# Performance work log

Hardware: AMD Instinct MI355X
Metric: run time of the kernel (lower is better)

## Reference

```python
import jax, jax.numpy as jnp
import numpy as np

ALPHA = 0.2      # LeakyReLU negative slope
NEG_INF = -9e15  # mask value from the original module
EPS = 1e-8


def setup_inputs() -> dict:
    key = jax.random.key(0)
    k1, k2, k3, k4 = jax.random.split(key, 4)
    B, N, F_in, F_out = 8, 2048, 128, 64
    h = jax.random.normal(k1, (B, N, F_in), dtype=jnp.float32)
    u = jax.random.uniform(k2, (B, N, N), dtype=jnp.float32)
    adj = jnp.where(u > 0.9, u, 0.0)
    adj = jnp.maximum(adj, jnp.eye(N, dtype=jnp.float32)[None])
    # Xavier-uniform with gain 1.414 as in the torch init
    gain = 1.414
    bW = gain * np.sqrt(6.0 / (F_in + F_out))
    W = jax.random.uniform(k3, (F_in, F_out), jnp.float32, -bW, bW)
    ba = gain * np.sqrt(6.0 / (2 * F_out + 1))
    a = jax.random.uniform(k4, (2 * F_out, 1), jnp.float32, -ba, ba)
    return {"h": h, "adj": adj, "W": W, "a": a}


def reference(h, adj, W, a):
    # h: [B,N,Fin], adj: [B,N,N], W: [Fin,Fout], a: [2*Fout,1]
    F_out = W.shape[1]
    Wh = jnp.einsum('bnf,fo->bno', h, W)                      # [B,N,Fout]
    # Split-projection equivalent of cat([Wh_i, Wh_j]) @ a:
    # e[b,i,j] = leaky(Wh[b,i]@a1 + Wh[b,j]@a2)
    a1 = a[:F_out, 0]
    a2 = a[F_out:, 0]
    e = jax.nn.leaky_relu(
        (Wh @ a1)[:, :, None] + (Wh @ a2)[:, None, :],        # [B,N,N]
        negative_slope=ALPHA,
    )
    att = jnp.where(adj > 0, e, NEG_INF)
    att = jax.nn.softmax(att, axis=2)
    att = att * adj
    att = att / (jnp.sum(att, axis=2, keepdims=True) + EPS)
    h_prime = jnp.einsum('bij,bjo->bio', att, Wh)             # [B,N,Fout]
    return jax.nn.elu(h_prime)                                # concat=True -> ELU
```

## Files before the change

### kernel.cpp

```cpp
#include <hip/hip_runtime.h>
#include <hip/hip_bf16.h>
#include <stdint.h>

#define LRELU_ALPHA 0.2f

constexpr int BB = 8, NN = 2048, FIN = 128, FOUT = 64;

typedef __attribute__((ext_vector_type(8))) short short8;
typedef __attribute__((ext_vector_type(4))) float f32x4;

__device__ __forceinline__ ushort bf16rn(float f) {
    __hip_bfloat16 h = __float2bfloat16(f);
    return *reinterpret_cast<ushort*>(&h);
}

#define HS 132
__global__ __launch_bounds__(256) void k_gemm_hw(const float* __restrict__ h,
                                                 const float* __restrict__ W,
                                                 const float* __restrict__ a,
                                                 ushort* __restrict__ WhP,
                                                 float* __restrict__ s1,
                                                 float* __restrict__ s2,
                                                 float* __restrict__ pmax) {
    __shared__ float hs[64 * HS];
    __shared__ float smax[16];
    const int tid = threadIdx.x;
    const int base = blockIdx.x * 64;

    #pragma unroll
    for (int rep = 0; rep < 8; ++rep) {
        int flat4 = rep * 256 + tid;
        int row = flat4 >> 5, k4 = flat4 & 31;
        float4 v = *reinterpret_cast<const float4*>(h + (size_t)(base + row) * FIN + k4 * 4);
        *reinterpret_cast<float4*>(&hs[row * HS + k4 * 4]) = v;
    }
    __syncthreads();

    const int tr = tid >> 4;
    const int tc = tid & 15;
    float acc[4][4] = {};
    for (int k = 0; k < FIN; ++k) {
        float4 wv = *reinterpret_cast<const float4*>(W + (size_t)k * FOUT + tc * 4);
        #pragma unroll
        for (int r = 0; r < 4; ++r) {
            float hv = hs[(tr * 4 + r) * HS + k];
            acc[r][0] = fmaf(hv, wv.x, acc[r][0]);
            acc[r][1] = fmaf(hv, wv.y, acc[r][1]);
            acc[r][2] = fmaf(hv, wv.z, acc[r][2]);
            acc[r][3] = fmaf(hv, wv.w, acc[r][3]);
        }
    }

    const int b = base >> 11;
    const int jbase = base & 2047;
    #pragma unroll
    for (int r = 0; r < 4; ++r) {
        const int jloc = jbase + tr * 4 + r;
        const int e = jloc & 7;
        const int kgrp = (jloc >> 3) & 3;
        const int jblk = jloc >> 5;
        #pragma unroll
        for (int c = 0; c < 4; ++c) {
            const int col = tc * 4 + c;
            size_t off = ((((size_t)b * 64 + jblk) * 4 + (col >> 4)) * 64 + kgrp * 16 + (col & 15)) * 8 + e;
            WhP[off] = bf16rn(acc[r][c]);
        }
    }

    float a1c[4], a2c[4];
    #pragma unroll
    for (int c = 0; c < 4; ++c) {
        a1c[c] = a[tc * 4 + c];
        a2c[c] = a[FOUT + tc * 4 + c];
    }
    float maxp2 = -3.4e38f;
    #pragma unroll
    for (int r = 0; r < 4; ++r) {
        float p1 = acc[r][0] * a1c[0] + acc[r][1] * a1c[1] + acc[r][2] * a1c[2] + acc[r][3] * a1c[3];
        float p2 = acc[r][0] * a2c[0] + acc[r][1] * a2c[1] + acc[r][2] * a2c[2] + acc[r][3] * a2c[3];
        #pragma unroll
        for (int off = 1; off < 16; off <<= 1) {
            p1 += __shfl_xor(p1, off);
            p2 += __shfl_xor(p2, off);
        }
        if (tc == 0) {
            s1[base + tr * 4 + r] = p1;
            s2[base + tr * 4 + r] = p2;
            maxp2 = fmaxf(maxp2, p2);
        }
    }
    if (tc == 0) smax[tr] = maxp2;
    __syncthreads();
    if (tid == 0) {
        float m = smax[0];
        #pragma unroll
        for (int i = 1; i < 16; ++i) m = fmaxf(m, smax[i]);
        pmax[blockIdx.x] = m;
    }
}

struct Tile {
    float4 a0, a1;
    float4 v0, v1;
    short8 b0, b1, b2, b3;
};

__device__ __forceinline__ void proc8(const Tile& T, float s1i, float c,
                                      float& Sp, short8& af) {
    const float aa[8] = {T.a0.x, T.a0.y, T.a0.z, T.a0.w, T.a1.x, T.a1.y, T.a1.z, T.a1.w};
    const float ss[8] = {T.v0.x, T.v0.y, T.v0.z, T.v0.w, T.v1.x, T.v1.y, T.v1.z, T.v1.w};
    #pragma unroll
    for (int e = 0; e < 8; ++e) {
        float ev = s1i + ss[e];
        ev = ev > 0.f ? ev : LRELU_ALPHA * ev;
        float ex = __expf(ev - c);
        float wv = aa[e] > 0.f ? aa[e] * ex : 0.f;
        ushort ub = bf16rn(wv);
        Sp += __uint_as_float((uint32_t)ub << 16);
        af[e] = (short)ub;
    }
}

__global__ __launch_bounds__(256) void k_attn(const float* __restrict__ adj,
                                              const ushort* __restrict__ WhP,
                                              const float* __restrict__ s1,
                                              const float* __restrict__ s2,
                                              const float* __restrict__ pmax,
                                              float* __restrict__ out) {
    const int tid = threadIdx.x;
    const int l = tid & 63, w = tid >> 6;
    const int li = l & 15, lk = l >> 4;
    const int blk = blockIdx.x;
    const int b = blk >> 5;
    const int rowbase = blk * 64 + w * 16;
    const int row_i = rowbase + li;

    float m = -3.4e38f;
    #pragma unroll
    for (int t = 0; t < 4; ++t) m = fmaxf(m, pmax[l + 64 * t]);
    #pragma unroll
    for (int off = 32; off > 0; off >>= 1) m = fmaxf(m, __shfl_xor(m, off));

    const float s1i = s1[row_i];
    const float cp = s1i + m;
    const float c = cp > 0.f ? cp : LRELU_ALPHA * cp;

    const float* __restrict__ adjp = adj + (size_t)row_i * NN + lk * 8;
    const float* __restrict__ s2p  = s2 + (size_t)b * NN + lk * 8;
    const ushort* __restrict__ whp = WhP + (size_t)b * (64 * 4 * 64 * 8) + l * 8;

    f32x4 acc0 = {0.f, 0.f, 0.f, 0.f};
    f32x4 acc1 = {0.f, 0.f, 0.f, 0.f};
    f32x4 acc2 = {0.f, 0.f, 0.f, 0.f};
    f32x4 acc3 = {0.f, 0.f, 0.f, 0.f};
    float Sp = 0.f;

#define LOADT(T, jb) do {                                                     \
        (T).a0 = *reinterpret_cast<const float4*>(adjp + (jb) * 32);          \
        (T).a1 = *reinterpret_cast<const float4*>(adjp + (jb) * 32 + 4);      \
        (T).v0 = *reinterpret_cast<const float4*>(s2p + (jb) * 32);           \
        (T).v1 = *reinterpret_cast<const float4*>(s2p + (jb) * 32 + 4);       \
        const ushort* p_ = whp + (jb) * 2048;                                 \
        (T).b0 = *reinterpret_cast<const short8*>(p_);                        \
        (T).b1 = *reinterpret_cast<const short8*>(p_ + 512);                  \
        (T).b2 = *reinterpret_cast<const short8*>(p_ + 1024);                 \
        (T).b3 = *reinterpret_cast<const short8*>(p_ + 1536);                 \
    } while (0)

#define COMPUTE(T) do {                                                       \
        short8 af;                                                            \
        proc8((T), s1i, c, Sp, af);                                           \
        acc0 = __builtin_amdgcn_mfma_f32_16x16x32_bf16(af, (T).b0, acc0, 0, 0, 0); \
        acc1 = __builtin_amdgcn_mfma_f32_16x16x32_bf16(af, (T).b1, acc1, 0, 0, 0); \
        acc2 = __builtin_amdgcn_mfma_f32_16x16x32_bf16(af, (T).b2, acc2, 0, 0, 0); \
        acc3 = __builtin_amdgcn_mfma_f32_16x16x32_bf16(af, (T).b3, acc3, 0, 0, 0); \
    } while (0)

    Tile t0, t1;
    LOADT(t0, 0);
    LOADT(t1, 1);
    for (int jb = 0; jb < 64; jb += 2) {
        Tile n0, n1;
        if (jb + 2 < 64) {
            LOADT(n0, jb + 2);
            LOADT(n1, jb + 3);
        }
        COMPUTE(t0);
        COMPUTE(t1);
        t0 = n0;
        t1 = n1;
    }

    float Sred = Sp;
    Sred += __shfl_xor(Sred, 16);
    Sred += __shfl_xor(Sred, 32);

    const f32x4 accs[4] = {acc0, acc1, acc2, acc3};
    #pragma unroll
    for (int r = 0; r < 4; ++r) {
        const int drow = lk * 4 + r;
        float Sr = __int_as_float(__builtin_amdgcn_ds_bpermute(drow * 4, __float_as_int(Sred)));
        float inv = 1.0f / Sr;
        #pragma unroll
        for (int tt = 0; tt < 4; ++tt) {
            float o = accs[tt][r] * inv;
            o = o > 0.f ? o : expm1f(o);
            out[(size_t)(rowbase + drow) * FOUT + tt * 16 + li] = o;
        }
    }
#undef LOADT
#undef COMPUTE
}

extern "C" void kernel_launch(void* const* d_in, const int* in_sizes, int n_in,
                              void* d_out, int out_size, void* d_ws, size_t ws_size,
                              hipStream_t stream) {
    (void)in_sizes; (void)n_in; (void)out_size; (void)ws_size;
    const float* h   = (const float*)d_in[0];
    const float* adj = (const float*)d_in[1];
    const float* W   = (const float*)d_in[2];
    const float* a   = (const float*)d_in[3];
    float* out = (float*)d_out;

    ushort* WhP = (ushort*)d_ws;
    float* s1w  = (float*)(WhP + (size_t)BB * NN * FOUT);
    float* s2w  = s1w + (size_t)BB * NN;
    float* pmaxw = s2w + (size_t)BB * NN;

    k_gemm_hw<<<BB * NN / 64, 256, 0, stream>>>(h, W, a, WhP, s1w, s2w, pmaxw);
    k_attn<<<BB * NN / 64, 256, 0, stream>>>(adj, WhP, s1w, s2w, pmaxw, out);
}
```

Measured before the change: 53.55 us.

## Split attention j-range across waves with LDS reduction and finer-grained blocks

```diff
diff --git a/kernel.cpp b/kernel.cpp
--- a/kernel.cpp
+++ b/kernel.cpp
@@ -3,8 +3,11 @@
 #include <stdint.h>
 
 #define LRELU_ALPHA 0.2f
+#define L2E 1.44269504f
 
 constexpr int BB = 8, NN = 2048, FIN = 128, FOUT = 64;
+constexpr int GEMM_ROWS = 32;
+constexpr int NBLK_G = BB * NN / GEMM_ROWS;
 
 typedef __attribute__((ext_vector_type(8))) short short8;
 typedef __attribute__((ext_vector_type(4))) float f32x4;
@@ -22,13 +25,13 @@
                                                  float* __restrict__ s1,
                                                  float* __restrict__ s2,
                                                  float* __restrict__ pmax) {
-    __shared__ float hs[64 * HS];
+    __shared__ float hs[GEMM_ROWS * HS];
     __shared__ float smax[16];
     const int tid = threadIdx.x;
-    const int base = blockIdx.x * 64;
-
-    #pragma unroll
-    for (int rep = 0; rep < 8; ++rep) {
+    const int base = blockIdx.x * GEMM_ROWS;
+
+    #pragma unroll
+    for (int rep = 0; rep < 4; ++rep) {
         int flat4 = rep * 256 + tid;
         int row = flat4 >> 5, k4 = flat4 & 31;
         float4 v = *reinterpret_cast<const float4*>(h + (size_t)(base + row) * FIN + k4 * 4);
@@ -38,12 +41,13 @@
 
     const int tr = tid >> 4;
     const int tc = tid & 15;
-    float acc[4][4] = {};
+    float acc[2][4] = {};
+    #pragma unroll 4
     for (int k = 0; k < FIN; ++k) {
         float4 wv = *reinterpret_cast<const float4*>(W + (size_t)k * FOUT + tc * 4);
         #pragma unroll
-        for (int r = 0; r < 4; ++r) {
-            float hv = hs[(tr * 4 + r) * HS + k];
+        for (int r = 0; r < 2; ++r) {
+            float hv = hs[(tr * 2 + r) * HS + k];
             acc[r][0] = fmaf(hv, wv.x, acc[r][0]);
             acc[r][1] = fmaf(hv, wv.y, acc[r][1]);
             acc[r][2] = fmaf(hv, wv.z, acc[r][2]);
@@ -54,8 +58,8 @@
     const int b = base >> 11;
     const int jbase = base & 2047;
     #pragma unroll
-    for (int r = 0; r < 4; ++r) {
-        const int jloc = jbase + tr * 4 + r;
+    for (int r = 0; r < 2; ++r) {
+        const int jloc = jbase + tr * 2 + r;
         const int e = jloc & 7;
         const int kgrp = (jloc >> 3) & 3;
         const int jblk = jloc >> 5;
@@ -75,7 +79,7 @@
     }
     float maxp2 = -3.4e38f;
     #pragma unroll
-    for (int r = 0; r < 4; ++r) {
+    for (int r = 0; r < 2; ++r) {
         float p1 = acc[r][0] * a1c[0] + acc[r][1] * a1c[1] + acc[r][2] * a1c[2] + acc[r][3] * a1c[3];
         float p2 = acc[r][0] * a2c[0] + acc[r][1] * a2c[1] + acc[r][2] * a2c[2] + acc[r][3] * a2c[3];
         #pragma unroll
@@ -84,8 +88,8 @@
             p2 += __shfl_xor(p2, off);
         }
         if (tc == 0) {
-            s1[base + tr * 4 + r] = p1;
-            s2[base + tr * 4 + r] = p2;
+            s1[base + tr * 2 + r] = p1;
+            s2[base + tr * 2 + r] = p2;
             maxp2 = fmaxf(maxp2, p2);
         }
     }
@@ -99,55 +103,37 @@
     }
 }
 
-struct Tile {
-    float4 a0, a1;
-    float4 v0, v1;
-    short8 b0, b1, b2, b3;
-};
-
-__device__ __forceinline__ void proc8(const Tile& T, float s1i, float c,
-                                      float& Sp, short8& af) {
-    const float aa[8] = {T.a0.x, T.a0.y, T.a0.z, T.a0.w, T.a1.x, T.a1.y, T.a1.z, T.a1.w};
-    const float ss[8] = {T.v0.x, T.v0.y, T.v0.z, T.v0.w, T.v1.x, T.v1.y, T.v1.z, T.v1.w};
-    #pragma unroll
-    for (int e = 0; e < 8; ++e) {
-        float ev = s1i + ss[e];
-        ev = ev > 0.f ? ev : LRELU_ALPHA * ev;
-        float ex = __expf(ev - c);
-        float wv = aa[e] > 0.f ? aa[e] * ex : 0.f;
-        ushort ub = bf16rn(wv);
-        Sp += __uint_as_float((uint32_t)ub << 16);
-        af[e] = (short)ub;
-    }
-}
-
-__global__ __launch_bounds__(256) void k_attn(const float* __restrict__ adj,
-                                              const ushort* __restrict__ WhP,
-                                              const float* __restrict__ s1,
-                                              const float* __restrict__ s2,
-                                              const float* __restrict__ pmax,
-                                              float* __restrict__ out) {
+__global__ __launch_bounds__(256, 4) void k_attn(const float* __restrict__ adj,
+                                                 const ushort* __restrict__ WhP,
+                                                 const float* __restrict__ s1,
+                                                 const float* __restrict__ s2,
+                                                 const float* __restrict__ pmax,
+                                                 float* __restrict__ out) {
+    __shared__ float lacc[4][16][68];
+    __shared__ float lS[4][16];
+
     const int tid = threadIdx.x;
     const int l = tid & 63, w = tid >> 6;
     const int li = l & 15, lk = l >> 4;
     const int blk = blockIdx.x;
-    const int b = blk >> 5;
-    const int rowbase = blk * 64 + w * 16;
+    const int b = blk >> 7;
+    const int rowbase = blk * 16;
     const int row_i = rowbase + li;
 
     float m = -3.4e38f;
     #pragma unroll
-    for (int t = 0; t < 4; ++t) m = fmaxf(m, pmax[l + 64 * t]);
+    for (int t = 0; t < 8; ++t) m = fmaxf(m, pmax[l + 64 * t]);
     #pragma unroll
     for (int off = 32; off > 0; off >>= 1) m = fmaxf(m, __shfl_xor(m, off));
 
     const float s1i = s1[row_i];
     const float cp = s1i + m;
-    const float c = cp > 0.f ? cp : LRELU_ALPHA * cp;
-
-    const float* __restrict__ adjp = adj + (size_t)row_i * NN + lk * 8;
-    const float* __restrict__ s2p  = s2 + (size_t)b * NN + lk * 8;
-    const ushort* __restrict__ whp = WhP + (size_t)b * (64 * 4 * 64 * 8) + l * 8;
+    const float c = fmaxf(cp, LRELU_ALPHA * cp);
+    const float cL = c * L2E;
+
+    const float* __restrict__ adjp = adj + (size_t)row_i * NN + w * 512 + lk * 8;
+    const float* __restrict__ s2p  = s2 + (size_t)b * NN + w * 512 + lk * 8;
+    const ushort* __restrict__ whp = WhP + (size_t)b * 131072 + (size_t)(w * 16) * 2048 + l * 8;
 
     f32x4 acc0 = {0.f, 0.f, 0.f, 0.f};
     f32x4 acc1 = {0.f, 0.f, 0.f, 0.f};
@@ -155,61 +141,71 @@
     f32x4 acc3 = {0.f, 0.f, 0.f, 0.f};
     float Sp = 0.f;
 
-#define LOADT(T, jb) do {                                                     \
-        (T).a0 = *reinterpret_cast<const float4*>(adjp + (jb) * 32);          \
-        (T).a1 = *reinterpret_cast<const float4*>(adjp + (jb) * 32 + 4);      \
-        (T).v0 = *reinterpret_cast<const float4*>(s2p + (jb) * 32);           \
-        (T).v1 = *reinterpret_cast<const float4*>(s2p + (jb) * 32 + 4);       \
-        const ushort* p_ = whp + (jb) * 2048;                                 \
-        (T).b0 = *reinterpret_cast<const short8*>(p_);                        \
-        (T).b1 = *reinterpret_cast<const short8*>(p_ + 512);                  \
-        (T).b2 = *reinterpret_cast<const short8*>(p_ + 1024);                 \
-        (T).b3 = *reinterpret_cast<const short8*>(p_ + 1536);                 \
-    } while (0)
-
-#define COMPUTE(T) do {                                                       \
-        short8 af;                                                            \
-        proc8((T), s1i, c, Sp, af);                                           \
-        acc0 = __builtin_amdgcn_mfma_f32_16x16x32_bf16(af, (T).b0, acc0, 0, 0, 0); \
-        acc1 = __builtin_amdgcn_mfma_f32_16x16x32_bf16(af, (T).b1, acc1, 0, 0, 0); \
-        acc2 = __builtin_amdgcn_mfma_f32_16x16x32_bf16(af, (T).b2, acc2, 0, 0, 0); \
-        acc3 = __builtin_amdgcn_mfma_f32_16x16x32_bf16(af, (T).b3, acc3, 0, 0, 0); \
-    } while (0)
-
-    Tile t0, t1;
-    LOADT(t0, 0);
-    LOADT(t1, 1);
-    for (int jb = 0; jb < 64; jb += 2) {
-        Tile n0, n1;
-        if (jb + 2 < 64) {
-            LOADT(n0, jb + 2);
-            LOADT(n1, jb + 3);
-        }
-        COMPUTE(t0);
-        COMPUTE(t1);
-        t0 = n0;
-        t1 = n1;
+    float4 pa[2][2];
+    pa[0][0] = *reinterpret_cast<const float4*>(adjp);
+    pa[0][1] = *reinterpret_cast<const float4*>(adjp + 4);
+    pa[1][0] = *reinterpret_cast<const float4*>(adjp + 32);
+    pa[1][1] = *reinterpret_cast<const float4*>(adjp + 36);
+
+    #pragma unroll
+    for (int t = 0; t < 16; ++t) {
+        const float4 a0 = pa[t & 1][0];
+        const float4 a1 = pa[t & 1][1];
+        if (t + 2 < 16) {
+            pa[t & 1][0] = *reinterpret_cast<const float4*>(adjp + (t + 2) * 32);
+            pa[t & 1][1] = *reinterpret_cast<const float4*>(adjp + (t + 2) * 32 + 4);
+        }
+        const float4 v0 = *reinterpret_cast<const float4*>(s2p + t * 32);
+        const float4 v1 = *reinterpret_cast<const float4*>(s2p + t * 32 + 4);
+        const ushort* p_ = whp + t * 2048;
+        const short8 b0 = *reinterpret_cast<const short8*>(p_);
+        const short8 b1 = *reinterpret_cast<const short8*>(p_ + 512);
+        const short8 b2 = *reinterpret_cast<const short8*>(p_ + 1024);
+        const short8 b3 = *reinterpret_cast<const short8*>(p_ + 1536);
+
+        const float aa[8] = {a0.x, a0.y, a0.z, a0.w, a1.x, a1.y, a1.z, a1.w};
+        const float ss[8] = {v0.x, v0.y, v0.z, v0.w, v1.x, v1.y, v1.z, v1.w};
+        short8 af;
+        #pragma unroll
+        for (int e = 0; e < 8; ++e) {
+            float ev = s1i + ss[e];
+            float lr = fmaxf(ev, LRELU_ALPHA * ev);
+            float ex = exp2f(fmaf(lr, L2E, -cL));
+            float wv = aa[e] * ex;
+            ushort ub = bf16rn(wv);
+            Sp += __uint_as_float((uint32_t)ub << 16);
+            af[e] = (short)ub;
+        }
+        acc0 = __builtin_amdgcn_mfma_f32_16x16x32_bf16(af, b0, acc0, 0, 0, 0);
+        acc1 = __builtin_amdgcn_mfma_f32_16x16x32_bf16(af, b1, acc1, 0, 0, 0);
+        acc2 = __builtin_amdgcn_mfma_f32_16x16x32_bf16(af, b2, acc2, 0, 0, 0);
+        acc3 = __builtin_amdgcn_mfma_f32_16x16x32_bf16(af, b3, acc3, 0, 0, 0);
     }
 
     float Sred = Sp;
     Sred += __shfl_xor(Sred, 16);
     Sred += __shfl_xor(Sred, 32);
+    if (l < 16) lS[w][li] = Sred;
 
     const f32x4 accs[4] = {acc0, acc1, acc2, acc3};
     #pragma unroll
-    for (int r = 0; r < 4; ++r) {
-        const int drow = lk * 4 + r;
-        float Sr = __int_as_float(__builtin_amdgcn_ds_bpermute(drow * 4, __float_as_int(Sred)));
-        float inv = 1.0f / Sr;
-        #pragma unroll
-        for (int tt = 0; tt < 4; ++tt) {
-            float o = accs[tt][r] * inv;
-            o = o > 0.f ? o : expm1f(o);
-            out[(size_t)(rowbase + drow) * FOUT + tt * 16 + li] = o;
-        }
-    }
-#undef LOADT
-#undef COMPUTE
+    for (int r = 0; r < 4; ++r)
+        #pragma unroll
+        for (int tt = 0; tt < 4; ++tt)
+            lacc[w][lk * 4 + r][tt * 16 + li] = accs[tt][r];
+
+    __syncthreads();
+
+    #pragma unroll
+    for (int q = 0; q < 4; ++q) {
+        const int idx = q * 256 + tid;
+        const int row = idx >> 6, col = idx & 63;
+        float v = lacc[0][row][col] + lacc[1][row][col] + lacc[2][row][col] + lacc[3][row][col];
+        float S = lS[0][row] + lS[1][row] + lS[2][row] + lS[3][row];
+        float o = v / S;
+        o = o > 0.f ? o : expm1f(o);
+        out[(size_t)(rowbase + row) * FOUT + col] = o;
+    }
 }
 
 extern "C" void kernel_launch(void* const* d_in, const int* in_sizes, int n_in,
@@ -227,6 +223,6 @@
     float* s2w  = s1w + (size_t)BB * NN;
     float* pmaxw = s2w + (size_t)BB * NN;
 
-    k_gemm_hw<<<BB * NN / 64, 256, 0, stream>>>(h, W, a, WhP, s1w, s2w, pmaxw);
-    k_attn<<<BB * NN / 64, 256, 0, stream>>>(adj, WhP, s1w, s2w, pmaxw, out);
-}
+    k_gemm_hw<<<NBLK_G, 256, 0, stream>>>(h, W, a, WhP, s1w, s2w, pmaxw);
+    k_attn<<<BB * NN / 16, 256, 0, stream>>>(adj, WhP, s1w, s2w, pmaxw, out);
+}
```

Result: faster. 52.19 us (-2.5%).
